# Performance work log

Hardware: AMD Instinct MI355X
Metric: run time of the kernel (lower is better)

## Reference

```python
import jax, jax.numpy as jnp
import numpy as np

COUNTS = [1536, 8192, 16384, 24576, 12288, 1024, 512, 512, 256, 128, 128]
OFFS = np.concatenate([[0], np.cumsum(COUNTS)]).astype(int).tolist()
N = OFFS[-1]          # 65536 atoms total, sorted by degree
MAX_DEG = 10
BATCH = 2048          # fixed GraphGather batch size
F_IN = 75
GC = 256
DENSE = 512
N_TASKS = 12
N_CLASSES = 2
BN_EPS = 1e-3         # keras BatchNormalization default epsilon


def _graph_conv(x, deg_adjs, w0, wself, wneigh, b):
    # deepchem GraphConv: per-degree (self @ Wself + sum_neighbors @ Wneigh + b), relu
    outs = [x[OFFS[0]:OFFS[1]] @ w0 + b[0]]  # degree-0 atoms: self transform only
    for d in range(1, MAX_DEG + 1):
        self_atoms = x[OFFS[d]:OFFS[d + 1]]            # [n_d, F]
        neigh = x[deg_adjs[d - 1]].sum(axis=1)         # gather [n_d, d, F] -> sum -> [n_d, F]
        outs.append(self_atoms @ wself[d - 1] + neigh @ wneigh[d - 1] + b[d])
    return jax.nn.relu(jnp.concatenate(outs, axis=0))


def _graph_pool(x, deg_adjs):
    # deepchem GraphPool: elementwise max over {self} U neighbors, per degree
    outs = [x[OFFS[0]:OFFS[1]]]  # degree-0 atoms pass through
    for d in range(1, MAX_DEG + 1):
        self_atoms = x[OFFS[d]:OFFS[d + 1]]
        outs.append(jnp.maximum(self_atoms, x[deg_adjs[d - 1]].max(axis=1)))
    return jnp.concatenate(outs, axis=0)


def _bn(x, g, bta, m, v):
    # inference-mode BatchNormalization (training=False -> moving stats)
    return g * (x - m) * jax.lax.rsqrt(v + BN_EPS) + bta


def setup_inputs():
    key = jax.random.key(0)
    ks = iter(jax.random.split(key, 64))
    inp = {}
    inp["atom_features"] = jax.random.normal(next(ks), (N, F_IN), jnp.float32)
    inp["degree_slice"] = jnp.asarray(
        np.stack([np.array(OFFS[:-1]), np.array(COUNTS)], axis=1), jnp.int32)
    # each molecule gets exactly N/BATCH atoms so no GraphGather segment is empty
    inp["membership"] = jax.random.permutation(
        next(ks), jnp.arange(N, dtype=jnp.int32) % BATCH)
    inp["n_samples"] = BATCH
    for d in range(1, MAX_DEG + 1):
        inp["deg_adj_%d" % d] = jax.random.randint(
            next(ks), (COUNTS[d], d), 0, N, jnp.int32)

    def lin(k, fi, fo):
        return jax.random.normal(k, (fi, fo), jnp.float32) * np.float32(1.0 / np.sqrt(fi))

    for li, fi in [(1, F_IN), (2, GC)]:
        inp["gc%d_w0" % li] = lin(next(ks), fi, GC)
        inp["gc%d_wself" % li] = jnp.stack([lin(next(ks), fi, GC) for _ in range(MAX_DEG)])
        inp["gc%d_wneigh" % li] = jnp.stack([lin(next(ks), fi, GC) for _ in range(MAX_DEG)])
        inp["gc%d_b" % li] = jnp.zeros((MAX_DEG + 1, GC), jnp.float32)
    for bi, dim in [(1, GC), (2, GC), (3, DENSE)]:
        inp["bn%d_gamma" % bi] = jnp.ones((dim,), jnp.float32)
        inp["bn%d_beta" % bi] = jnp.zeros((dim,), jnp.float32)
        inp["bn%d_mean" % bi] = jnp.zeros((dim,), jnp.float32)
        inp["bn%d_var" % bi] = jnp.ones((dim,), jnp.float32)
    inp["dense_w"] = lin(next(ks), GC, DENSE)
    inp["dense_b"] = jnp.zeros((DENSE,), jnp.float32)
    inp["out_w"] = lin(next(ks), 2 * DENSE, N_TASKS * N_CLASSES)
    inp["out_b"] = jnp.zeros((N_TASKS * N_CLASSES,), jnp.float32)
    return inp


def reference(atom_features, degree_slice, membership, n_samples,
              deg_adj_1, deg_adj_2, deg_adj_3, deg_adj_4, deg_adj_5,
              deg_adj_6, deg_adj_7, deg_adj_8, deg_adj_9, deg_adj_10,
              gc1_w0, gc1_wself, gc1_wneigh, gc1_b,
              gc2_w0, gc2_wself, gc2_wneigh, gc2_b,
              bn1_gamma, bn1_beta, bn1_mean, bn1_var,
              bn2_gamma, bn2_beta, bn2_mean, bn2_var,
              bn3_gamma, bn3_beta, bn3_mean, bn3_var,
              dense_w, dense_b, out_w, out_b):
    deg_adjs = [deg_adj_1, deg_adj_2, deg_adj_3, deg_adj_4, deg_adj_5,
                deg_adj_6, deg_adj_7, deg_adj_8, deg_adj_9, deg_adj_10]
    h = _graph_conv(atom_features, deg_adjs, gc1_w0, gc1_wself, gc1_wneigh, gc1_b)
    h = _bn(h, bn1_gamma, bn1_beta, bn1_mean, bn1_var)
    h = _graph_pool(h, deg_adjs)
    h = _graph_conv(h, deg_adjs, gc2_w0, gc2_wself, gc2_wneigh, gc2_b)
    h = _bn(h, bn2_gamma, bn2_beta, bn2_mean, bn2_var)
    h = _graph_pool(h, deg_adjs)
    h = jax.nn.relu(h @ dense_w + dense_b)
    h = _bn(h, bn3_gamma, bn3_beta, bn3_mean, bn3_var)
    # GraphGather: tanh(concat(segment_sum, segment_max))
    ssum = jax.ops.segment_sum(h, membership, num_segments=BATCH)
    smax = jax.ops.segment_max(h, membership, num_segments=BATCH)
    fp = jnp.tanh(jnp.concatenate([ssum, smax], axis=1))   # [BATCH, 2*DENSE]
    logits = (fp @ out_w + out_b).reshape(BATCH, N_TASKS, N_CLASSES)[:n_samples]
    probs = jax.nn.softmax(logits, axis=-1)
    return probs, logits, fp
```

## Files before the change

### kernel.cpp

```cpp
#include <hip/hip_runtime.h>
#include <hip/hip_fp16.h>
#include <math.h>

#define NATOMS 65536

typedef _Float16 f16_t;
typedef __attribute__((ext_vector_type(8))) _Float16 half8;
typedef __attribute__((ext_vector_type(4))) float f32x4;

__constant__ int c_offs[12] = {0,1536,9728,26112,50688,62976,64000,64512,65024,65280,65408,65536};

struct Adj { const int* p[10]; };

__device__ __forceinline__ int seg_of(int row) {
    int s = 0;
#pragma unroll
    for (int i = 1; i <= 10; ++i) s += (row >= c_offs[i]) ? 1 : 0;
    return s;
}

__device__ __forceinline__ void glds16(const f16_t* g, f16_t* l) {
    __builtin_amdgcn_global_load_lds(
        (const __attribute__((address_space(1))) unsigned int*)g,
        (__attribute__((address_space(3))) unsigned int*)l,
        16, 0, 0);
}

__device__ __forceinline__ half8 max8(half8 a, half8 b) {
    half8 r;
#pragma unroll
    for (int e = 0; e < 8; ++e) r[e] = (a[e] >= b[e]) ? a[e] : b[e];
    return r;
}


__global__ void pack_cvt(const float* __restrict__ g1w0, const float* __restrict__ g1ws,
                         const float* __restrict__ g1wn,
                         const float* __restrict__ g2w0, const float* __restrict__ g2ws,
                         const float* __restrict__ g2wn,
                         const float* __restrict__ dw, const float* __restrict__ ow,
                         f16_t* __restrict__ W1p, f16_t* __restrict__ W2p,
                         f16_t* __restrict__ Wdp, f16_t* __restrict__ Wop,
                         int* __restrict__ counts,
                         const float* __restrict__ xf, f16_t* __restrict__ xq) {
    if (blockIdx.x >= 8384) {
        int idx = (blockIdx.x - 8384) * 256 + threadIdx.x;
        int r = idx / 12;
        int cc = idx - r * 12;
        int c = cc << 3;
        f16_t o[8];
#pragma unroll
        for (int e = 0; e < 8; ++e)
            o[e] = (c + e < 75) ? (f16_t)xf[(size_t)r*75 + c + e] : (f16_t)0.f;
        *(uint4*)(xq + (size_t)r*96 + c) = *(uint4*)o;
        return;
    }
    int idx = blockIdx.x * 256 + threadIdx.x;
    if (idx < 2048) counts[idx] = 0;
    if (idx < 540672) {
        int j = idx & 7, lane = (idx >> 3) & 63;
        int kb = (idx >> 9) % 6;
        int rest = idx / (512 * 6);
        int ni = rest & 15, s = rest >> 4;
        int k = kb * 32 + (lane >> 4) * 8 + j;
        int n = ni * 16 + (lane & 15);
        float v = 0.f;
        if (k < 75) v = (s == 0) ? g1w0[k*256 + n] : g1ws[((s-1)*75 + k)*256 + n];
        else if (k >= 96 && k < 171 && s > 0) v = g1wn[((s-1)*75 + (k-96))*256 + n];
        W1p[idx] = (f16_t)v;
    } else if (idx < 1982464) {
        int i2 = idx - 540672;
        int j = i2 & 7, lane = (i2 >> 3) & 63;
        int kb = (i2 >> 9) & 15;
        int rest = i2 >> 13;
        int ni = rest & 15, s = rest >> 4;
        int k = kb * 32 + (lane >> 4) * 8 + j;
        int n = ni * 16 + (lane & 15);
        float v = 0.f;
        if (k < 256) v = (s == 0) ? g2w0[k*256 + n] : g2ws[((s-1)*256 + k)*256 + n];
        else if (s > 0) v = g2wn[((s-1)*256 + (k-256))*256 + n];
        W2p[i2] = (f16_t)v;
    } else if (idx < 2113536) {
        int i2 = idx - 1982464;
        int j = i2 & 7, lane = (i2 >> 3) & 63;
        int kb = (i2 >> 9) & 7;
        int ni = (i2 >> 12) & 31;
        int k = kb * 32 + (lane >> 4) * 8 + j;
        int n = ni * 16 + (lane & 15);
        Wdp[i2] = (f16_t)dw[(size_t)k*512 + n];
    } else {
        int i2 = idx - 2113536;
        int j = i2 & 7, lane = (i2 >> 3) & 63;
        int kb = (i2 >> 9) & 31;
        int ni = i2 >> 14;
        int k = kb * 32 + (lane >> 4) * 8 + j;
        int n = ni * 16 + (lane & 15);
        Wop[i2] = (n < 24) ? (f16_t)ow[k*24 + n] : (f16_t)0.f;
    }
}

template<int D, int LD>
__device__ __forceinline__ void gathD(float* v, const f16_t* __restrict__ src,
                                      const int* __restrict__ ap, int c) {
    int rows[D];
#pragma unroll
    for (int j = 0; j < D; ++j) rows[j] = ap[j];
    uint4 raw[D];
#pragma unroll
    for (int j = 0; j < D; ++j) raw[j] = *(const uint4*)(src + (size_t)rows[j]*LD + c);
#pragma unroll
    for (int j = 0; j < D; ++j) {
        const f16_t* u = (const f16_t*)&raw[j];
#pragma unroll
        for (int e = 0; e < 8; ++e) v[e] += (float)u[e];
    }
}

template<int LD>
__device__ __forceinline__ void gath_sum(float* v, const f16_t* __restrict__ src,
                                         const int* __restrict__ ap, int s, int c) {
    switch (s) {
        case 1:  gathD<1,LD>(v,src,ap,c);  break;
        case 2:  gathD<2,LD>(v,src,ap,c);  break;
        case 3:  gathD<3,LD>(v,src,ap,c);  break;
        case 4:  gathD<4,LD>(v,src,ap,c);  break;
        case 5:  gathD<5,LD>(v,src,ap,c);  break;
        case 6:  gathD<6,LD>(v,src,ap,c);  break;
        case 7:  gathD<7,LD>(v,src,ap,c);  break;
        case 8:  gathD<8,LD>(v,src,ap,c);  break;
        case 9:  gathD<9,LD>(v,src,ap,c);  break;
        case 10: gathD<10,LD>(v,src,ap,c); break;
        default: break;
    }
}

template<int D, int LD>
__device__ __forceinline__ void gathD_pk(half8& v, const f16_t* __restrict__ src,
                                         const int* __restrict__ ap, int c) {
    int rows[D];
#pragma unroll
    for (int j = 0; j < D; ++j) rows[j] = ap[j];
    half8 raw[D];
#pragma unroll
    for (int j = 0; j < D; ++j) raw[j] = *(const half8*)(src + (size_t)rows[j]*LD + c);
#pragma unroll
    for (int j = 0; j < D; ++j) v = max8(v, raw[j]);
}

template<int LD>
__device__ __forceinline__ void gath_max(half8& v, const f16_t* __restrict__ src,
                                         const int* __restrict__ ap, int s, int c) {
    switch (s) {
        case 1:  gathD_pk<1,LD>(v,src,ap,c);  break;
        case 2:  gathD_pk<2,LD>(v,src,ap,c);  break;
        case 3:  gathD_pk<3,LD>(v,src,ap,c);  break;
        case 4:  gathD_pk<4,LD>(v,src,ap,c);  break;
        case 5:  gathD_pk<5,LD>(v,src,ap,c);  break;
        case 6:  gathD_pk<6,LD>(v,src,ap,c);  break;
        case 7:  gathD_pk<7,LD>(v,src,ap,c);  break;
        case 8:  gathD_pk<8,LD>(v,src,ap,c);  break;
        case 9:  gathD_pk<9,LD>(v,src,ap,c);  break;
        case 10: gathD_pk<10,LD>(v,src,ap,c); break;
        default: break;
    }
}

__global__ __launch_bounds__(256) void nbsum_sc(const f16_t* __restrict__ xq,
                                                f16_t* __restrict__ NBX, Adj adj,
                                                const int* __restrict__ mem,
                                                int* __restrict__ counts,
                                                int* __restrict__ slots) {
    if (blockIdx.x >= 3072) {
        int i = (blockIdx.x - 3072) * 256 + threadIdx.x;
        int s = mem[i];
        int p = atomicAdd(&counts[s], 1);
        if (p < 32) slots[s*32 + p] = i;
        return;
    }
    int idx = blockIdx.x * 256 + threadIdx.x;
    int r = (int)((unsigned)idx / 12u);
    int cc = idx - r * 12;
    int c = cc << 3;
    int s = seg_of(r);
    float v[8];
#pragma unroll
    for (int e = 0; e < 8; ++e) v[e] = 0.f;
    if (s > 0)
        gath_sum<96>(v, xq, adj.p[s-1] + (size_t)(r - c_offs[s]) * s, s, c);
    f16_t o[8];
#pragma unroll
    for (int e = 0; e < 8; ++e) o[e] = (f16_t)v[e];
    *(uint4*)(NBX + (size_t)(r>>4)*1536 + (c>>5)*512 + ((c>>3)&3)*128 + (r&15)*8) = *(uint4*)o;
}

template<bool BLOB>
__global__ __launch_bounds__(256) void pool_k(const f16_t* __restrict__ H,
                                              f16_t* __restrict__ P, Adj adj) {
    int idx = blockIdx.x * 256 + threadIdx.x;
    int r = idx >> 5;
    int c = (idx & 31) << 3;
    int s = seg_of(r);
    half8 v = *(const half8*)(H + (size_t)r*256 + c);
    if (s > 0)
        gath_max<256>(v, H, adj.p[s-1] + (size_t)(r - c_offs[s]) * s, s, c);
    if (BLOB)
        *(half8*)(P + (size_t)(r>>4)*4096 + (c>>5)*512 + ((c>>3)&3)*128 + (r&15)*8) = v;
    else
        *(half8*)(P + (size_t)r*256 + c) = v;
}

__global__ __launch_bounds__(256) void nbsum_k(const f16_t* __restrict__ P,
                                               f16_t* __restrict__ NB, Adj adj) {
    int idx = blockIdx.x * 256 + threadIdx.x;
    int r = idx >> 5;
    int c = (idx & 31) << 3;
    int s = seg_of(r);
    float v[8];
#pragma unroll
    for (int e = 0; e < 8; ++e) v[e] = 0.f;
    if (s > 0)
        gath_sum<256>(v, P, adj.p[s-1] + (size_t)(r - c_offs[s]) * s, s, c);
    f16_t o[8];
#pragma unroll
    for (int e = 0; e < 8; ++e) o[e] = (f16_t)v[e];
    *(uint4*)(NB + (size_t)(r>>4)*4096 + (c>>5)*512 + ((c>>3)&3)*128 + (r&15)*8) = *(uint4*)o;
}

template<int K, int KSPLIT, int LDA, int NKBA1, int N, int NY, bool SEG>
__global__ __launch_bounds__(256)
void gemm_rm(const f16_t* __restrict__ A0, const f16_t* __restrict__ A1,
             const f16_t* __restrict__ Wp,
             const float* __restrict__ bias,
             const float* __restrict__ bng, const float* __restrict__ bnb,
             const float* __restrict__ bnm, const float* __restrict__ bnv,
             f16_t* __restrict__ C)
{
    constexpr int NKB = K / 32;
    constexpr int KSPB = KSPLIT / 32;
    constexpr int NNT = N / 16;
    __shared__ char smem[32768];
    f16_t* sm = (f16_t*)smem;
    f16_t* eps = (f16_t*)smem;

    const int t = threadIdx.x;
    const int lane = t & 63, wave = t >> 6;
    const int wm = wave >> 1, wn = wave & 1;
    const int quad = lane >> 4, l16 = lane & 15;
    const int id = blockIdx.x;
    const int xcd = id & 7;
    const int jj = id >> 3;
    const int xi = jj / NY;
    const int y  = jj - xi * NY;
    const int r0 = (xi * 8 + xcd) * 128;
    const int n0 = y * 128;
    const int seg = SEG ? seg_of(r0) : 0;
    const int nbase = n0 >> 4;
    const int rtg = r0 >> 4;

    f32x4 acc[4][4];
#pragma unroll
    for (int mi = 0; mi < 4; ++mi)
#pragma unroll
        for (int ni = 0; ni < 4; ++ni) acc[mi][ni] = (f32x4){0.f,0.f,0.f,0.f};

    size_t aoff[2];
#pragma unroll
    for (int i = 0; i < 2; ++i)
        aoff[i] = (size_t)(r0 + (wave*2 + i)*16 + l16) * LDA + quad*8;
    size_t bbase[2];
#pragma unroll
    for (int i = 0; i < 2; ++i)
        bbase[i] = ((size_t)(seg*NNT + nbase + wave*2 + i) * NKB) * 512 + lane*8;

#pragma unroll
    for (int kbp = 0; kbp < NKB/2; ++kbp) {
#pragma unroll
        for (int u = 0; u < 2; ++u) {
            const int kb = kbp*2 + u;
#pragma unroll
            for (int i = 0; i < 2; ++i) {
                const int rt = wave*2 + i;
                if (kb < KSPB) {
                    glds16(A0 + (size_t)kb*32 + aoff[i], sm + u*4096 + rt*512);
                } else {
                    glds16(A1 + ((size_t)(rtg + rt)*NKBA1 + (kb - KSPB))*512 + lane*8,
                           sm + u*4096 + rt*512);
                }
                glds16(Wp + bbase[i] + (size_t)kb*512, sm + 8192 + u*4096 + rt*512);
            }
        }
        __syncthreads();
#pragma unroll
        for (int u = 0; u < 2; ++u) {
            half8 a[4], b[4];
#pragma unroll
            for (int mi = 0; mi < 4; ++mi)
                a[mi] = *(const half8*)(sm + u*4096 + (wm*4 + mi)*512 + lane*8);
#pragma unroll
            for (int ni = 0; ni < 4; ++ni)
                b[ni] = *(const half8*)(sm + 8192 + u*4096 + (wn*4 + ni)*512 + lane*8);
#pragma unroll
            for (int mi = 0; mi < 4; ++mi)
#pragma unroll
                for (int ni = 0; ni < 4; ++ni)
                    acc[mi][ni] = __builtin_amdgcn_mfma_f32_16x16x32_f16(a[mi], b[ni], acc[mi][ni], 0, 0, 0);
        }
        __syncthreads();
    }

#pragma unroll
    for (int p = 0; p < 2; ++p) {
        if (wm == p) {
#pragma unroll
            for (int ni = 0; ni < 4; ++ni) {
                const int lcol = (wn*4 + ni)*16 + l16;
                const int col = n0 + lcol;
                const float scale = bng[col] * rsqrtf(bnv[col] + 1e-3f);
                const float shift = bnb[col] - bnm[col] * scale;
                const float bv = bias[(SEG ? seg*N : 0) + col];
#pragma unroll
                for (int mi = 0; mi < 4; ++mi) {
                    const int lrowb = mi*16 + quad*4;
#pragma unroll
                    for (int r = 0; r < 4; ++r) {
                        float v = acc[mi][ni][r] + bv;
                        v = fmaxf(v, 0.f);
                        v = fmaf(v, scale, shift);
                        eps[(lrowb + r)*136 + lcol] = (f16_t)v;
                    }
                }
            }
        }
        __syncthreads();
#pragma unroll
        for (int it = 0; it < 4; ++it) {
            int row = it*16 + (t >> 4);
            int ch  = t & 15;
            uint4 v = *(const uint4*)&eps[row*136 + ch*8];
            *(uint4*)(C + (size_t)(r0 + p*64 + row)*N + n0 + ch*8) = v;
        }
        __syncthreads();
    }
}

template<int NKB, int N, int NY>
__global__ __launch_bounds__(256)
void gemm_bl(const f16_t* __restrict__ A,
             const f16_t* __restrict__ Wp,
             const float* __restrict__ bias,
             const float* __restrict__ bng, const float* __restrict__ bnb,
             const float* __restrict__ bnm, const float* __restrict__ bnv,
             f16_t* __restrict__ C)
{
    constexpr int NNT = N / 16;
    __shared__ char smem[32768];
    f16_t* sm = (f16_t*)smem;
    f16_t* eps = (f16_t*)smem;

    const int t = threadIdx.x;
    const int lane = t & 63, wave = t >> 6;
    const int wm = wave >> 1, wn = wave & 1;
    const int quad = lane >> 4, l16 = lane & 15;
    const int id = blockIdx.x;
    const int xcd = id & 7;
    const int jj = id >> 3;
    const int xi = jj / NY;
    const int y  = jj - xi * NY;
    const int r0 = (xi * 8 + xcd) * 128;
    const int n0 = y * 128;
    const int nbase = n0 >> 4;
    const int rtg = r0 >> 4;

    f32x4 acc[4][4];
#pragma unroll
    for (int mi = 0; mi < 4; ++mi)
#pragma unroll
        for (int ni = 0; ni < 4; ++ni) acc[mi][ni] = (f32x4){0.f,0.f,0.f,0.f};

#pragma unroll
    for (int kbp = 0; kbp < NKB/2; ++kbp) {
#pragma unroll
        for (int u = 0; u < 2; ++u) {
            const int kb = kbp*2 + u;
#pragma unroll
            for (int i = 0; i < 2; ++i) {
                const int rt = wave*2 + i;
                glds16(A + ((size_t)(rtg + rt)*NKB + kb)*512 + lane*8, sm + u*4096 + rt*512);
                glds16(Wp + ((size_t)(nbase + rt)*NKB + kb)*512 + lane*8,
                       sm + 8192 + u*4096 + rt*512);
            }
        }
        __syncthreads();
#pragma unroll
        for (int u = 0; u < 2; ++u) {
            half8 a[4], b[4];
#pragma unroll
            for (int mi = 0; mi < 4; ++mi)
                a[mi] = *(const half8*)(sm + u*4096 + (wm*4 + mi)*512 + lane*8);
#pragma unroll
            for (int ni = 0; ni < 4; ++ni)
                b[ni] = *(const half8*)(sm + 8192 + u*4096 + (wn*4 + ni)*512 + lane*8);
#pragma unroll
            for (int mi = 0; mi < 4; ++mi)
#pragma unroll
                for (int ni = 0; ni < 4; ++ni)
                    acc[mi][ni] = __builtin_amdgcn_mfma_f32_16x16x32_f16(a[mi], b[ni], acc[mi][ni], 0, 0, 0);
        }
        __syncthreads();
    }

#pragma unroll
    for (int p = 0; p < 2; ++p) {
        if (wm == p) {
#pragma unroll
            for (int ni = 0; ni < 4; ++ni) {
                const int lcol = (wn*4 + ni)*16 + l16;
                const int col = n0 + lcol;
                const float scale = bng[col] * rsqrtf(bnv[col] + 1e-3f);
                const float shift = bnb[col] - bnm[col] * scale;
                const float bv = bias[col];
#pragma unroll
                for (int mi = 0; mi < 4; ++mi) {
                    const int lrowb = mi*16 + quad*4;
#pragma unroll
                    for (int r = 0; r < 4; ++r) {
                        float v = acc[mi][ni][r] + bv;
                        v = fmaxf(v, 0.f);
                        v = fmaf(v, scale, shift);
                        eps[(lrowb + r)*136 + lcol] = (f16_t)v;
                    }
                }
            }
        }
        __syncthreads();
#pragma unroll
        for (int it = 0; it < 4; ++it) {
            int row = it*16 + (t >> 4);
            int ch  = t & 15;
            uint4 v = *(const uint4*)&eps[row*136 + ch*8];
            *(uint4*)(C + (size_t)(r0 + p*64 + row)*N + n0 + ch*8) = v;
        }
        __syncthreads();
    }
}

__global__ __launch_bounds__(256)
void reduce_k(const f16_t* __restrict__ H3, const int* __restrict__ slots,
              float* __restrict__ fp) {
    __shared__ float shs[3][512];
    __shared__ float shm[3][512];
    int s = blockIdx.x;
    int t = threadIdx.x;
    int w = t >> 6, l = t & 63;
    int c = l * 8;
    const int* sl = slots + s*32 + w*8;
    float sm[8], mx[8];
#pragma unroll
    for (int e = 0; e < 8; ++e) { sm[e] = 0.f; mx[e] = -INFINITY; }
#pragma unroll
    for (int i = 0; i < 8; ++i) {
        int a = sl[i];
        uint4 raw = *(const uint4*)(H3 + (size_t)a*512 + c);
        const f16_t* u = (const f16_t*)&raw;
#pragma unroll
        for (int e = 0; e < 8; ++e) {
            float f = (float)u[e];
            sm[e] += f;
            mx[e] = fmaxf(mx[e], f);
        }
    }
    if (w) {
        *(float4*)&shs[w-1][c]   = *(float4*)&sm[0];
        *(float4*)&shs[w-1][c+4] = *(float4*)&sm[4];
        *(float4*)&shm[w-1][c]   = *(float4*)&mx[0];
        *(float4*)&shm[w-1][c+4] = *(float4*)&mx[4];
    }
    __syncthreads();
    if (w == 0) {
#pragma unroll
        for (int j = 0; j < 3; ++j)
#pragma unroll
            for (int e = 0; e < 8; ++e) {
                sm[e] += shs[j][c+e];
                mx[e] = fmaxf(mx[e], shm[j][c+e]);
            }
        float o1[8], o2[8];
#pragma unroll
        for (int e = 0; e < 8; ++e) {
            o1[e] = tanhf(sm[e]); o2[e] = tanhf(mx[e]);
        }
        float* fr = fp + (size_t)s*1024;
        *(float4*)(fr + c)       = *(float4*)&o1[0];
        *(float4*)(fr + c + 4)   = *(float4*)&o1[4];
        *(float4*)(fr + 512 + c)     = *(float4*)&o2[0];
        *(float4*)(fr + 512 + c + 4) = *(float4*)&o2[4];
    }
}

__global__ __launch_bounds__(64)
void final_mfma(const float* __restrict__ fp, const f16_t* __restrict__ Wop,
                const float* __restrict__ out_b,
                float* __restrict__ probs, float* __restrict__ logits) {
    const int t = threadIdx.x;
    const int lane = t & 63;
    const int quad = lane >> 4, l16 = lane & 15;
    const int r0 = blockIdx.x * 16;

    f32x4 acc[2];
#pragma unroll
    for (int ni = 0; ni < 2; ++ni) acc[ni] = (f32x4){0.f,0.f,0.f,0.f};

    const size_t rowoff = (size_t)(r0 + l16) * 1024 + quad*8;
    size_t boff[2];
#pragma unroll
    for (int ni = 0; ni < 2; ++ni)
        boff[ni] = (size_t)ni * 32 * 512 + lane*8;

    auto loadA = [&](half8& a, int kb) {
        const float* src = fp + rowoff + kb*32;
        float4 u0 = *(const float4*)(src);
        float4 u1 = *(const float4*)(src + 4);
        half8 h;
        h[0] = (f16_t)u0.x; h[1] = (f16_t)u0.y; h[2] = (f16_t)u0.z; h[3] = (f16_t)u0.w;
        h[4] = (f16_t)u1.x; h[5] = (f16_t)u1.y; h[6] = (f16_t)u1.z; h[7] = (f16_t)u1.w;
        a = h;
    };
    auto loadB = [&](half8* b, int kb) {
#pragma unroll
        for (int ni = 0; ni < 2; ++ni) b[ni] = *(const half8*)(Wop + boff[ni] + (size_t)kb*512);
    };
    auto domfma = [&](half8& a, half8* b) {
#pragma unroll
        for (int ni = 0; ni < 2; ++ni)
            acc[ni] = __builtin_amdgcn_mfma_f32_16x16x32_f16(a, b[ni], acc[ni], 0, 0, 0);
    };

    half8 a0, b0[2], a1, b1[2];
    loadA(a0, 0); loadB(b0, 0);
#pragma unroll
    for (int kb = 0; kb < 32; kb += 2) {
        loadA(a1, kb + 1); loadB(b1, kb + 1);
        domfma(a0, b0);
        if (kb + 2 < 32) { loadA(a0, kb + 2); loadB(b0, kb + 2); }
        domfma(a1, b1);
    }

#pragma unroll
    for (int ni = 0; ni < 2; ++ni) {
        const int c = ni*16 + l16;
        const bool ok = (c < 24);
        const float bv = ok ? out_b[c] : 0.f;
#pragma unroll
        for (int r = 0; r < 4; ++r) {
            float lg = acc[ni][r] + bv;
            float lp = __shfl_xor(lg, 1);
            float m = fmaxf(lg, lp);
            float e  = expf(lg - m);
            float ep = expf(lp - m);
            float pr = e / (e + ep);
            if (ok) {
                int row = r0 + quad*4 + r;
                logits[(size_t)row*24 + c] = lg;
                probs[(size_t)row*24 + c]  = pr;
            }
        }
    }
}

extern "C" void kernel_launch(void* const* d_in, const int* in_sizes, int n_in,
                              void* d_out, int out_size, void* d_ws, size_t ws_size,
                              hipStream_t stream) {
    const float* atom       = (const float*)d_in[0];
    const int*   membership = (const int*)  d_in[2];
    Adj adj;
    for (int d = 0; d < 10; ++d) adj.p[d] = (const int*)d_in[4+d];
    const float* gc1_w0     = (const float*)d_in[14];
    const float* gc1_wself  = (const float*)d_in[15];
    const float* gc1_wneigh = (const float*)d_in[16];
    const float* gc1_b      = (const float*)d_in[17];
    const float* gc2_w0     = (const float*)d_in[18];
    const float* gc2_wself  = (const float*)d_in[19];
    const float* gc2_wneigh = (const float*)d_in[20];
    const float* gc2_b      = (const float*)d_in[21];
    const float* bn1g = (const float*)d_in[22]; const float* bn1b = (const float*)d_in[23];
    const float* bn1m = (const float*)d_in[24]; const float* bn1v = (const float*)d_in[25];
    const float* bn2g = (const float*)d_in[26]; const float* bn2b = (const float*)d_in[27];
    const float* bn2m = (const float*)d_in[28]; const float* bn2v = (const float*)d_in[29];
    const float* bn3g = (const float*)d_in[30]; const float* bn3b = (const float*)d_in[31];
    const float* bn3m = (const float*)d_in[32]; const float* bn3v = (const float*)d_in[33];
    const float* dense_w = (const float*)d_in[34];
    const float* dense_b = (const float*)d_in[35];
    const float* out_w   = (const float*)d_in[36];
    const float* out_b   = (const float*)d_in[37];

    f16_t* wsb = (f16_t*)d_ws;
    f16_t* xq    = wsb;
    f16_t* NBX   = wsb + 6291456;
    f16_t* H1b   = wsb + 12582912;
    f16_t* P1rm  = wsb + 29360128;
    f16_t* NB2b  = wsb + 46137344;
    f16_t* H2b   = H1b;
    f16_t* P2bl  = NB2b;
    f16_t* H3b   = H1b;
    f16_t* W1p   = wsb + 62914560;
    f16_t* W2p   = wsb + 63455232;
    f16_t* Wdp   = wsb + 64897024;
    f16_t* Wop   = wsb + 65028096;
    int*  counts = (int*)(wsb + 65060864);
    int*  slots  = counts + 2048;

    float* outp   = (float*)d_out;
    float* probs  = outp;
    float* logits = outp + 49152;
    float* fp     = outp + 98304;

    pack_cvt<<<11456, 256, 0, stream>>>(gc1_w0, gc1_wself, gc1_wneigh,
                                        gc2_w0, gc2_wself, gc2_wneigh,
                                        dense_w, out_w,
                                        W1p, W2p, Wdp, Wop, counts,
                                        atom, xq);

    nbsum_sc<<<3328, 256, 0, stream>>>(xq, NBX, adj, membership, counts, slots);
    gemm_rm<192,96,96,3,256,2,true><<<1024, 256, 0, stream>>>(
        xq, NBX, W1p, gc1_b, bn1g, bn1b, bn1m, bn1v, H1b);
    pool_k<false><<<(NATOMS*32)/256, 256, 0, stream>>>(H1b, P1rm, adj);

    nbsum_k<<<(NATOMS*32)/256, 256, 0, stream>>>(P1rm, NB2b, adj);
    gemm_rm<512,256,256,8,256,2,true><<<1024, 256, 0, stream>>>(
        P1rm, NB2b, W2p, gc2_b, bn2g, bn2b, bn2m, bn2v, H2b);
    pool_k<true><<<(NATOMS*32)/256, 256, 0, stream>>>(H2b, P2bl, adj);

    gemm_bl<8,512,4><<<2048, 256, 0, stream>>>(
        P2bl, Wdp, dense_b, bn3g, bn3b, bn3m, bn3v, H3b);

    reduce_k<<<2048, 256, 0, stream>>>(H3b, slots, fp);

    final_mfma<<<128, 64, 0, stream>>>(fp, Wop, out_b, probs, logits);
}
```

Before: 343.5 us.

## Replace 128x128 GEMMs with unified 256x256-tile double-buffered MFMA kernel

Merges the two GEMM kernels into a single template that computes 256x256 output tiles with 512 threads (8 waves), double-buffers the LDS staging so the next k-tile loads while the current one computes, and handles tiles that span two degree segments by reading the per-wave weight fragments straight from global memory. Larger tiles raise operand reuse and cut global/LDS traffic per FLOP. The cost is far fewer blocks (256 or 512), which leaves part of the 256 CUs idle. It also uses 128 KB of LDS per block and more accumulator registers, and the XCD-aware block mapping is dropped.

```diff
diff --git a/kernel.cpp b/kernel.cpp
--- a/kernel.cpp
+++ b/kernel.cpp
@@ -226,219 +226,146 @@
     *(uint4*)(NB + (size_t)(r>>4)*4096 + (c>>5)*512 + ((c>>3)&3)*128 + (r&15)*8) = *(uint4*)o;
 }
 
-template<int K, int KSPLIT, int LDA, int NKBA1, int N, int NY, bool SEG>
-__global__ __launch_bounds__(256)
-void gemm_rm(const f16_t* __restrict__ A0, const f16_t* __restrict__ A1,
+template<int NKB, int KSPB, int LDA, int NKBA1, int NY, int N, bool SEG>
+__global__ __launch_bounds__(512, 2)
+void gemm256(const f16_t* __restrict__ A0, const f16_t* __restrict__ A1,
              const f16_t* __restrict__ Wp,
              const float* __restrict__ bias,
              const float* __restrict__ bng, const float* __restrict__ bnb,
              const float* __restrict__ bnm, const float* __restrict__ bnv,
              f16_t* __restrict__ C)
 {
-    constexpr int NKB = K / 32;
-    constexpr int KSPB = KSPLIT / 32;
+    constexpr int NT  = NKB / 2;
     constexpr int NNT = N / 16;
-    __shared__ char smem[32768];
-    f16_t* sm = (f16_t*)smem;
-    f16_t* eps = (f16_t*)smem;
+    __shared__ f16_t sm[65536];
 
     const int t = threadIdx.x;
-    const int lane = t & 63, wave = t >> 6;
-    const int wm = wave >> 1, wn = wave & 1;
+    const int lane = t & 63, w = t >> 6;
+    const int wm = w >> 2, wn = w & 3;
     const int quad = lane >> 4, l16 = lane & 15;
     const int id = blockIdx.x;
-    const int xcd = id & 7;
-    const int jj = id >> 3;
-    const int xi = jj / NY;
-    const int y  = jj - xi * NY;
-    const int r0 = (xi * 8 + xcd) * 128;
-    const int n0 = y * 128;
-    const int seg = SEG ? seg_of(r0) : 0;
+    const int xi = id / NY, y = id - xi * NY;
+    const int r0 = xi * 256;
+    const int n0 = y * 256;
+    const int rtg = r0 >> 4;
     const int nbase = n0 >> 4;
-    const int rtg = r0 >> 4;
-
-    f32x4 acc[4][4];
-#pragma unroll
-    for (int mi = 0; mi < 4; ++mi)
+    const int segB = SEG ? seg_of(r0) : 0;
+    const bool strad = SEG && (seg_of(r0 + 255) != segB);
+    const int segw = SEG ? seg_of(r0 + wm*128) : 0;
+
+    f32x4 acc[8][4];
+#pragma unroll
+    for (int mi = 0; mi < 8; ++mi)
 #pragma unroll
         for (int ni = 0; ni < 4; ++ni) acc[mi][ni] = (f32x4){0.f,0.f,0.f,0.f};
 
     size_t aoff[2];
 #pragma unroll
     for (int i = 0; i < 2; ++i)
-        aoff[i] = (size_t)(r0 + (wave*2 + i)*16 + l16) * LDA + quad*8;
-    size_t bbase[2];
-#pragma unroll
-    for (int i = 0; i < 2; ++i)
-        bbase[i] = ((size_t)(seg*NNT + nbase + wave*2 + i) * NKB) * 512 + lane*8;
-
-#pragma unroll
-    for (int kbp = 0; kbp < NKB/2; ++kbp) {
-#pragma unroll
-        for (int u = 0; u < 2; ++u) {
-            const int kb = kbp*2 + u;
-#pragma unroll
-            for (int i = 0; i < 2; ++i) {
-                const int rt = wave*2 + i;
-                if (kb < KSPB) {
-                    glds16(A0 + (size_t)kb*32 + aoff[i], sm + u*4096 + rt*512);
+        aoff[i] = (size_t)(r0 + (w*2 + i)*16 + l16) * LDA + quad*8;
+
+    auto stage = [&](int kt, int buf) {
+        f16_t* bb = sm + buf*32768;
+#pragma unroll
+        for (int i = 0; i < 2; ++i) {
+            const int rt = w*2 + i;
+#pragma unroll
+            for (int kb2 = 0; kb2 < 2; ++kb2) {
+                const int kb = kt*2 + kb2;
+                if constexpr (KSPB > 0) {
+                    if (kb < KSPB)
+                        glds16(A0 + (size_t)kb*32 + aoff[i], bb + (rt*2 + kb2)*512);
+                    else
+                        glds16(A1 + ((size_t)(rtg + rt)*NKBA1 + (kb - KSPB))*512 + lane*8,
+                               bb + (rt*2 + kb2)*512);
                 } else {
-                    glds16(A1 + ((size_t)(rtg + rt)*NKBA1 + (kb - KSPB))*512 + lane*8,
-                           sm + u*4096 + rt*512);
+                    glds16(A1 + ((size_t)(rtg + rt)*NKBA1 + kb)*512 + lane*8,
+                           bb + (rt*2 + kb2)*512);
                 }
-                glds16(Wp + bbase[i] + (size_t)kb*512, sm + 8192 + u*4096 + rt*512);
+                glds16(Wp + ((size_t)(segB*NNT + nbase + rt)*NKB + kb)*512 + lane*8,
+                       bb + 16384 + (rt*2 + kb2)*512);
             }
         }
+    };
+
+    stage(0, 0);
+    __syncthreads();
+
+    for (int kt = 0; kt < NT; ++kt) {
+        const int buf = kt & 1;
+        if (kt + 1 < NT) stage(kt + 1, buf ^ 1);
+        const f16_t* bb = sm + buf*32768;
+
+        half8 bfr[4][2];
+        if (strad) {
+#pragma unroll
+            for (int ni = 0; ni < 4; ++ni)
+#pragma unroll
+                for (int kb2 = 0; kb2 < 2; ++kb2)
+                    bfr[ni][kb2] = *(const half8*)(Wp +
+                        ((size_t)(segw*NNT + nbase + wn*4 + ni)*NKB + kt*2 + kb2)*512 + lane*8);
+        } else {
+#pragma unroll
+            for (int ni = 0; ni < 4; ++ni)
+#pragma unroll
+                for (int kb2 = 0; kb2 < 2; ++kb2)
+                    bfr[ni][kb2] = *(const half8*)(bb + 16384 +
+                        ((wn*4 + ni)*2 + kb2)*512 + lane*8);
+        }
+
+#pragma unroll
+        for (int ph = 0; ph < 4; ++ph) {
+            half8 a[2][2];
+#pragma unroll
+            for (int m2 = 0; m2 < 2; ++m2)
+#pragma unroll
+                for (int kb2 = 0; kb2 < 2; ++kb2)
+                    a[m2][kb2] = *(const half8*)(bb +
+                        ((wm*8 + ph*2 + m2)*2 + kb2)*512 + lane*8);
+#pragma unroll
+            for (int m2 = 0; m2 < 2; ++m2)
+#pragma unroll
+                for (int ni = 0; ni < 4; ++ni)
+#pragma unroll
+                    for (int kb2 = 0; kb2 < 2; ++kb2)
+                        acc[ph*2 + m2][ni] = __builtin_amdgcn_mfma_f32_16x16x32_f16(
+                            a[m2][kb2], bfr[ni][kb2], acc[ph*2 + m2][ni], 0, 0, 0);
+        }
         __syncthreads();
-#pragma unroll
-        for (int u = 0; u < 2; ++u) {
-            half8 a[4], b[4];
-#pragma unroll
-            for (int mi = 0; mi < 4; ++mi)
-                a[mi] = *(const half8*)(sm + u*4096 + (wm*4 + mi)*512 + lane*8);
-#pragma unroll
-            for (int ni = 0; ni < 4; ++ni)
-                b[ni] = *(const half8*)(sm + 8192 + u*4096 + (wn*4 + ni)*512 + lane*8);
-#pragma unroll
-            for (int mi = 0; mi < 4; ++mi)
-#pragma unroll
-                for (int ni = 0; ni < 4; ++ni)
-                    acc[mi][ni] = __builtin_amdgcn_mfma_f32_16x16x32_f16(a[mi], b[ni], acc[mi][ni], 0, 0, 0);
-        }
-        __syncthreads();
-    }
-
-#pragma unroll
-    for (int p = 0; p < 2; ++p) {
-        if (wm == p) {
+    }
+
+    f16_t* eps = sm;
+#pragma unroll
+    for (int s = 0; s < 4; ++s) {
+        if (wm == (s >> 1)) {
 #pragma unroll
             for (int ni = 0; ni < 4; ++ni) {
-                const int lcol = (wn*4 + ni)*16 + l16;
+                const int lcol = wn*64 + ni*16 + l16;
                 const int col = n0 + lcol;
                 const float scale = bng[col] * rsqrtf(bnv[col] + 1e-3f);
                 const float shift = bnb[col] - bnm[col] * scale;
-                const float bv = bias[(SEG ? seg*N : 0) + col];
-#pragma unroll
-                for (int mi = 0; mi < 4; ++mi) {
-                    const int lrowb = mi*16 + quad*4;
-#pragma unroll
-                    for (int r = 0; r < 4; ++r) {
-                        float v = acc[mi][ni][r] + bv;
+                const float bv = bias[(SEG ? segw*N : 0) + col];
+#pragma unroll
+                for (int m2 = 0; m2 < 4; ++m2) {
+                    const int mi = (s & 1)*4 + m2;
+                    const int rowb = m2*16 + quad*4;
+#pragma unroll
+                    for (int rr = 0; rr < 4; ++rr) {
+                        float v = acc[mi][ni][rr] + bv;
                         v = fmaxf(v, 0.f);
                         v = fmaf(v, scale, shift);
-                        eps[(lrowb + r)*136 + lcol] = (f16_t)v;
+                        eps[(rowb + rr)*264 + lcol] = (f16_t)v;
                     }
                 }
             }
         }
         __syncthreads();
 #pragma unroll
-        for (int it = 0; it < 4; ++it) {
-            int row = it*16 + (t >> 4);
-            int ch  = t & 15;
-            uint4 v = *(const uint4*)&eps[row*136 + ch*8];
-            *(uint4*)(C + (size_t)(r0 + p*64 + row)*N + n0 + ch*8) = v;
-        }
-        __syncthreads();
-    }
-}
-
-template<int NKB, int N, int NY>
-__global__ __launch_bounds__(256)
-void gemm_bl(const f16_t* __restrict__ A,
-             const f16_t* __restrict__ Wp,
-             const float* __restrict__ bias,
-             const float* __restrict__ bng, const float* __restrict__ bnb,
-             const float* __restrict__ bnm, const float* __restrict__ bnv,
-             f16_t* __restrict__ C)
-{
-    constexpr int NNT = N / 16;
-    __shared__ char smem[32768];
-    f16_t* sm = (f16_t*)smem;
-    f16_t* eps = (f16_t*)smem;
-
-    const int t = threadIdx.x;
-    const int lane = t & 63, wave = t >> 6;
-    const int wm = wave >> 1, wn = wave & 1;
-    const int quad = lane >> 4, l16 = lane & 15;
-    const int id = blockIdx.x;
-    const int xcd = id & 7;
-    const int jj = id >> 3;
-    const int xi = jj / NY;
-    const int y  = jj - xi * NY;
-    const int r0 = (xi * 8 + xcd) * 128;
-    const int n0 = y * 128;
-    const int nbase = n0 >> 4;
-    const int rtg = r0 >> 4;
-
-    f32x4 acc[4][4];
-#pragma unroll
-    for (int mi = 0; mi < 4; ++mi)
-#pragma unroll
-        for (int ni = 0; ni < 4; ++ni) acc[mi][ni] = (f32x4){0.f,0.f,0.f,0.f};
-
-#pragma unroll
-    for (int kbp = 0; kbp < NKB/2; ++kbp) {
-#pragma unroll
-        for (int u = 0; u < 2; ++u) {
-            const int kb = kbp*2 + u;
-#pragma unroll
-            for (int i = 0; i < 2; ++i) {
-                const int rt = wave*2 + i;
-                glds16(A + ((size_t)(rtg + rt)*NKB + kb)*512 + lane*8, sm + u*4096 + rt*512);
-                glds16(Wp + ((size_t)(nbase + rt)*NKB + kb)*512 + lane*8,
-                       sm + 8192 + u*4096 + rt*512);
-            }
-        }
-        __syncthreads();
-#pragma unroll
-        for (int u = 0; u < 2; ++u) {
-            half8 a[4], b[4];
-#pragma unroll
-            for (int mi = 0; mi < 4; ++mi)
-                a[mi] = *(const half8*)(sm + u*4096 + (wm*4 + mi)*512 + lane*8);
-#pragma unroll
-            for (int ni = 0; ni < 4; ++ni)
-                b[ni] = *(const half8*)(sm + 8192 + u*4096 + (wn*4 + ni)*512 + lane*8);
-#pragma unroll
-            for (int mi = 0; mi < 4; ++mi)
-#pragma unroll
-                for (int ni = 0; ni < 4; ++ni)
-                    acc[mi][ni] = __builtin_amdgcn_mfma_f32_16x16x32_f16(a[mi], b[ni], acc[mi][ni], 0, 0, 0);
-        }
-        __syncthreads();
-    }
-
-#pragma unroll
-    for (int p = 0; p < 2; ++p) {
-        if (wm == p) {
-#pragma unroll
-            for (int ni = 0; ni < 4; ++ni) {
-                const int lcol = (wn*4 + ni)*16 + l16;
-                const int col = n0 + lcol;
-                const float scale = bng[col] * rsqrtf(bnv[col] + 1e-3f);
-                const float shift = bnb[col] - bnm[col] * scale;
-                const float bv = bias[col];
-#pragma unroll
-                for (int mi = 0; mi < 4; ++mi) {
-                    const int lrowb = mi*16 + quad*4;
-#pragma unroll
-                    for (int r = 0; r < 4; ++r) {
-                        float v = acc[mi][ni][r] + bv;
-                        v = fmaxf(v, 0.f);
-                        v = fmaf(v, scale, shift);
-                        eps[(lrowb + r)*136 + lcol] = (f16_t)v;
-                    }
-                }
-            }
-        }
-        __syncthreads();
-#pragma unroll
-        for (int it = 0; it < 4; ++it) {
-            int row = it*16 + (t >> 4);
-            int ch  = t & 15;
-            uint4 v = *(const uint4*)&eps[row*136 + ch*8];
-            *(uint4*)(C + (size_t)(r0 + p*64 + row)*N + n0 + ch*8) = v;
+        for (int k = 0; k < 4; ++k) {
+            int idx = k*512 + t;
+            int row = idx >> 5, ch = idx & 31;
+            *(uint4*)(C + (size_t)(r0 + s*64 + row)*N + n0 + ch*8) =
+                *(const uint4*)&eps[row*264 + ch*8];
         }
         __syncthreads();
     }
@@ -621,17 +548,17 @@
                                         atom, xq);
 
     nbsum_sc<<<3328, 256, 0, stream>>>(xq, NBX, adj, membership, counts, slots);
-    gemm_rm<192,96,96,3,256,2,true><<<1024, 256, 0, stream>>>(
+    gemm256<6,3,96,3,1,256,true><<<256, 512, 0, stream>>>(
         xq, NBX, W1p, gc1_b, bn1g, bn1b, bn1m, bn1v, H1b);
     pool_k<false><<<(NATOMS*32)/256, 256, 0, stream>>>(H1b, P1rm, adj);
 
     nbsum_k<<<(NATOMS*32)/256, 256, 0, stream>>>(P1rm, NB2b, adj);
-    gemm_rm<512,256,256,8,256,2,true><<<1024, 256, 0, stream>>>(
+    gemm256<16,8,256,8,1,256,true><<<256, 512, 0, stream>>>(
         P1rm, NB2b, W2p, gc2_b, bn2g, bn2b, bn2m, bn2v, H2b);
     pool_k<true><<<(NATOMS*32)/256, 256, 0, stream>>>(H2b, P2bl, adj);
 
-    gemm_bl<8,512,4><<<2048, 256, 0, stream>>>(
-        P2bl, Wdp, dense_b, bn3g, bn3b, bn3m, bn3v, H3b);
+    gemm256<8,0,1,8,2,512,false><<<512, 512, 0, stream>>>(
+        P2bl, P2bl, Wdp, dense_b, bn3g, bn3b, bn3m, bn3v, H3b);
 
     reduce_k<<<2048, 256, 0, stream>>>(H3b, slots, fp);
 
```

New measurement: 340.3 us. About the same (-0.9%).
